# Kernel optimization log

Measured on AMD Instinct MI355X. Metric: run time of the kernel, lower is better.

## Reference

```python
import jax, jax.numpy as jnp
import numpy as np

B, T, F, D, H = 16, 512, 32, 256, 256
EPS = 1e-5


def _layernorm(y, g, b):
    m = jnp.mean(y, axis=-1, keepdims=True)
    v = jnp.mean((y - m) ** 2, axis=-1, keepdims=True)
    return (y - m) / jnp.sqrt(v + EPS) * g + b


def setup_inputs() -> dict:
    key = jax.random.key(0)
    ks = jax.random.split(key, 24)
    s = lambda fan_in: 1.0 / np.sqrt(fan_in)
    u = lambda k, shape, fan_in: jax.random.uniform(k, shape, jnp.float32, -s(fan_in), s(fan_in))
    return {
        "x": jax.random.normal(ks[0], (B, T, F), jnp.float32),
        # per-feature Linear(1, D), stacked over F
        "proj_w": u(ks[1], (F, D), 1),
        "proj_b": u(ks[2], (F, D), 1),
        # per-feature scorer GRN(D, H, 1), stacked over F
        "sc_fc1_w": u(ks[3], (F, H, D), D),
        "sc_fc1_b": u(ks[4], (F, H), D),
        "sc_fc2_w": u(ks[5], (F, 1, H), H),
        "sc_fc2_b": u(ks[6], (F, 1), H),
        "sc_gate_w": u(ks[7], (F, 1, 1), 1),
        "sc_gate_b": u(ks[8], (F, 1), 1),
        "sc_skip_w": u(ks[9], (F, 1, D), D),
        "sc_skip_b": u(ks[10], (F, 1), D),
        "sc_ln_g": jnp.ones((F, 1), jnp.float32),
        "sc_ln_b": jnp.zeros((F, 1), jnp.float32),
        # post GRN(D, H, D); in_dim == out_dim -> skip is identity
        "post_fc1_w": u(ks[11], (H, D), D),
        "post_fc1_b": u(ks[12], (H,), D),
        "post_fc2_w": u(ks[13], (D, H), H),
        "post_fc2_b": u(ks[14], (D,), H),
        "post_gate_w": u(ks[15], (D, D), D),
        "post_gate_b": u(ks[16], (D,), D),
        "post_ln_g": jnp.ones((D,), jnp.float32),
        "post_ln_b": jnp.zeros((D,), jnp.float32),
    }


def reference(x, proj_w, proj_b, sc_fc1_w, sc_fc1_b, sc_fc2_w, sc_fc2_b,
              sc_gate_w, sc_gate_b, sc_skip_w, sc_skip_b, sc_ln_g, sc_ln_b,
              post_fc1_w, post_fc1_b, post_fc2_w, post_fc2_b,
              post_gate_w, post_gate_b, post_ln_g, post_ln_b):
    # per-feature embedding: Linear(1 -> D), batched over F
    # E: [B, T, F, D]
    E = x[..., None] * proj_w[None, None] + proj_b[None, None]

    # per-feature scorer GRN(D, H, 1), all F at once
    h = jax.nn.elu(jnp.einsum("btfd,fhd->btfh", E, sc_fc1_w) + sc_fc1_b)
    h = jnp.einsum("btfh,foh->btfo", h, sc_fc2_w) + sc_fc2_b  # [B,T,F,1]
    g = jax.nn.sigmoid(jnp.einsum("btfo,fpo->btfp", h, sc_gate_w) + sc_gate_b)
    skip = jnp.einsum("btfd,fod->btfo", E, sc_skip_w) + sc_skip_b
    y = g * h + (1.0 - g) * skip
    S = _layernorm(y, sc_ln_g, sc_ln_b)  # [B,T,F,1] (last dim size 1)

    # softmax over features, weighted mixture
    W = jax.nn.softmax(S, axis=2)
    mix = jnp.sum(E * W, axis=2)  # [B,T,D]

    # post GRN(D, H, D), skip = identity
    h2 = jax.nn.elu(mix @ post_fc1_w.T + post_fc1_b)
    h2 = h2 @ post_fc2_w.T + post_fc2_b
    g2 = jax.nn.sigmoid(h2 @ post_gate_w.T + post_gate_b)
    y2 = g2 * h2 + (1.0 - g2) * mix
    return _layernorm(y2, post_ln_g, post_ln_b)
```

## Files before the change

### kernel.cpp

```cpp
#include <hip/hip_runtime.h>
#include <hip/hip_bf16.h>
#include <math.h>


typedef __bf16 bf16;
typedef __bf16 bf16x8 __attribute__((ext_vector_type(8)));
typedef __bf16 bf16x4 __attribute__((ext_vector_type(4)));
typedef float f32x4 __attribute__((ext_vector_type(4)));

#define NTOK 8192
#define D_   256
#define F_   32

#define OFF_C      512
#define OFF_WPROJT 2048
#define OFF_FC1    32768
#define OFF_FC2    163840
#define OFF_GATE   294912

__global__ __launch_bounds__(256) void vsn_prep(
    const float* __restrict__ proj_w, const float* __restrict__ proj_b,
    const float* __restrict__ sc_ln_b,
    const float* __restrict__ w1, const float* __restrict__ w2,
    const float* __restrict__ w3,
    float* __restrict__ wsC, bf16* __restrict__ wsWT,
    bf16* __restrict__ o1, bf16* __restrict__ o2, bf16* __restrict__ o3)
{
  const int blk = blockIdx.x;
  if (blk < 64) {
    int idx = blk * 256 + threadIdx.x;
    {
      float4 a = ((const float4*)w1)[idx];
      bf16x4 b = {(bf16)a.x, (bf16)a.y, (bf16)a.z, (bf16)a.w};
      ((bf16x4*)o1)[idx] = b;
    }
    {
      float4 a = ((const float4*)w2)[idx];
      bf16x4 b = {(bf16)a.x, (bf16)a.y, (bf16)a.z, (bf16)a.w};
      ((bf16x4*)o2)[idx] = b;
    }
    {
      float4 a = ((const float4*)w3)[idx];
      bf16x4 b = {(bf16)a.x, (bf16)a.y, (bf16)a.z, (bf16)a.w};
      ((bf16x4*)o3)[idx] = b;
    }
  } else {
    const int d = threadIdx.x;
    float wv[F_];
    float mx = -3.0e38f;
    #pragma unroll
    for (int f = 0; f < F_; f++) { wv[f] = sc_ln_b[f]; mx = fmaxf(mx, wv[f]); }
    float se = 0.0f;
    #pragma unroll
    for (int f = 0; f < F_; f++) { wv[f] = __expf(wv[f] - mx); se += wv[f]; }
    float inv = 1.0f / se;
    float acc = 0.0f;
    #pragma unroll
    for (int f = 0; f < F_; f++) {
      float wf = wv[f] * inv;
      acc += wf * proj_b[f * D_ + d];
      wsWT[d * F_ + f] = (bf16)(wf * proj_w[f * D_ + d]);
    }
    wsC[d] = acc;
  }
}

__global__ __launch_bounds__(256, 2) void vsn_main(
    const float* __restrict__ x,
    const float* __restrict__ wsC,
    const bf16* __restrict__ WT,
    const bf16* __restrict__ FC1, const float* __restrict__ fc1_b,
    const bf16* __restrict__ FC2, const float* __restrict__ fc2_b,
    const bf16* __restrict__ GATE, const float* __restrict__ gate_b,
    const float* __restrict__ ln_g, const float* __restrict__ ln_b,
    float* __restrict__ out)
{
  __shared__ bf16  sAct[16][264];
  __shared__ float sY[16][260];

  const int tid  = threadIdx.x;
  const int w    = tid >> 6;
  const int lane = tid & 63;
  const int lm   = lane & 15;
  const int lq   = lane >> 4;
  const int j0   = w * 4;
  const int tok0 = blockIdx.x * 16;

  const float* xp = x + (size_t)(tok0 + lm) * F_ + lq * 8;
  float4 x0 = *(const float4*)xp;
  float4 x1 = *(const float4*)(xp + 4);
  bf16x8 a0 = {(bf16)x0.x, (bf16)x0.y, (bf16)x0.z, (bf16)x0.w,
               (bf16)x1.x, (bf16)x1.y, (bf16)x1.z, (bf16)x1.w};
  f32x4 mixf[4];
  #pragma unroll
  for (int jj = 0; jj < 4; jj++) {
    int n = (j0 + jj) * 16 + lm;
    float cv = wsC[n];
    f32x4 acc = {cv, cv, cv, cv};
    bf16x8 b = *(const bf16x8*)(WT + n * F_ + lq * 8);
    acc = __builtin_amdgcn_mfma_f32_16x16x32_bf16(a0, b, acc, 0, 0, 0);
    mixf[jj] = acc;
    #pragma unroll
    for (int r = 0; r < 4; r++) sAct[lq * 4 + r][n] = (bf16)acc[r];
  }
  __syncthreads();

  bf16x8 af[8];
  auto loadA = [&]() {
    #pragma unroll
    for (int ks = 0; ks < 8; ks++)
      af[ks] = *(const bf16x8*)(&sAct[lm][ks * 32 + lq * 8]);
  };
  auto gemmB = [&](const bf16* __restrict__ W, f32x4* acc) {
    bf16x8 bb[8];
    const bf16* wp = W + (size_t)(j0 * 16 + lm) * 256 + lq * 8;
    #pragma unroll
    for (int ks = 0; ks < 8; ks++) bb[ks] = *(const bf16x8*)(wp + ks * 32);
    #pragma unroll
    for (int jj = 0; jj < 4; jj++) {
      bf16x8 bn[8];
      if (jj < 3) {
        const bf16* wn = W + (size_t)((j0 + jj + 1) * 16 + lm) * 256 + lq * 8;
        #pragma unroll
        for (int ks = 0; ks < 8; ks++) bn[ks] = *(const bf16x8*)(wn + ks * 32);
      }
      f32x4 a = {0.f, 0.f, 0.f, 0.f};
      acc[jj] = a;
      #pragma unroll
      for (int ks = 0; ks < 8; ks++)
        acc[jj] = __builtin_amdgcn_mfma_f32_16x16x32_bf16(af[ks], bb[ks], acc[jj], 0, 0, 0);
      if (jj < 3) {
        #pragma unroll
        for (int ks = 0; ks < 8; ks++) bb[ks] = bn[ks];
      }
    }
  };

  loadA();
  __syncthreads();
  {
    f32x4 acc[4];
    gemmB(FC1, acc);
    #pragma unroll
    for (int jj = 0; jj < 4; jj++) {
      int n = (j0 + jj) * 16 + lm;
      float bias = fc1_b[n];
      #pragma unroll
      for (int r = 0; r < 4; r++) {
        float v = acc[jj][r] + bias;
        v = (v > 0.0f) ? v : (__expf(v) - 1.0f);
        sAct[lq * 4 + r][n] = (bf16)v;
      }
    }
  }
  __syncthreads();

  f32x4 h2f[4];
  loadA();
  __syncthreads();
  {
    f32x4 acc[4];
    gemmB(FC2, acc);
    #pragma unroll
    for (int jj = 0; jj < 4; jj++) {
      int n = (j0 + jj) * 16 + lm;
      float bias = fc2_b[n];
      #pragma unroll
      for (int r = 0; r < 4; r++) {
        float v = acc[jj][r] + bias;
        h2f[jj][r] = v;
        sAct[lq * 4 + r][n] = (bf16)v;
      }
    }
  }
  __syncthreads();

  loadA();
  __syncthreads();
  {
    f32x4 acc[4];
    gemmB(GATE, acc);
    #pragma unroll
    for (int jj = 0; jj < 4; jj++) {
      int n = (j0 + jj) * 16 + lm;
      float bias = gate_b[n];
      #pragma unroll
      for (int r = 0; r < 4; r++) {
        float s = acc[jj][r] + bias;
        float g = 1.0f / (1.0f + __expf(-s));
        sY[lq * 4 + r][n] = g * h2f[jj][r] + (1.0f - g) * mixf[jj][r];
      }
    }
  }
  __syncthreads();

  {
    const int t = w * 4 + lq;
    float4 yv[4];
    #pragma unroll
    for (int i = 0; i < 4; i++)
      yv[i] = *(const float4*)(&sY[t][lm * 4 + i * 64]);
    const float inv_d = 1.0f / 256.0f;
    float s = 0.0f;
    #pragma unroll
    for (int i = 0; i < 4; i++) s += yv[i].x + yv[i].y + yv[i].z + yv[i].w;
    #pragma unroll
    for (int off = 1; off < 16; off <<= 1) s += __shfl_xor(s, off);
    float mean = s * inv_d;
    float q = 0.0f;
    #pragma unroll
    for (int i = 0; i < 4; i++) {
      float d0 = yv[i].x - mean, d1 = yv[i].y - mean,
            d2 = yv[i].z - mean, d3 = yv[i].w - mean;
      q += d0 * d0 + d1 * d1 + d2 * d2 + d3 * d3;
    }
    #pragma unroll
    for (int off = 1; off < 16; off <<= 1) q += __shfl_xor(q, off);
    float rstd = rsqrtf(q * inv_d + 1e-5f);
    #pragma unroll
    for (int i = 0; i < 4; i++) {
      int n = lm * 4 + i * 64;
      float4 gv = *(const float4*)(ln_g + n);
      float4 bv = *(const float4*)(ln_b + n);
      float4 o;
      o.x = (yv[i].x - mean) * rstd * gv.x + bv.x;
      o.y = (yv[i].y - mean) * rstd * gv.y + bv.y;
      o.z = (yv[i].z - mean) * rstd * gv.z + bv.z;
      o.w = (yv[i].w - mean) * rstd * gv.w + bv.w;
      *(float4*)(out + (size_t)(tok0 + t) * D_ + n) = o;
    }
  }
}

extern "C" void kernel_launch(void* const* d_in, const int* in_sizes, int n_in,
                              void* d_out, int out_size, void* d_ws, size_t ws_size,
                              hipStream_t stream) {
  (void)in_sizes; (void)n_in; (void)ws_size; (void)out_size;
  const float* x      = (const float*)d_in[0];
  const float* proj_w = (const float*)d_in[1];
  const float* proj_b = (const float*)d_in[2];
  const float* sclnb  = (const float*)d_in[12];
  const float* fc1w   = (const float*)d_in[13];
  const float* fc1b   = (const float*)d_in[14];
  const float* fc2w   = (const float*)d_in[15];
  const float* fc2b   = (const float*)d_in[16];
  const float* gw     = (const float*)d_in[17];
  const float* gb     = (const float*)d_in[18];
  const float* lng    = (const float*)d_in[19];
  const float* lnb    = (const float*)d_in[20];

  char* ws = (char*)d_ws;
  float* wsC   = (float*)(ws + OFF_C);
  bf16*  wsWT  = (bf16*)(ws + OFF_WPROJT);
  bf16*  bFC1  = (bf16*)(ws + OFF_FC1);
  bf16*  bFC2  = (bf16*)(ws + OFF_FC2);
  bf16*  bGATE = (bf16*)(ws + OFF_GATE);

  vsn_prep<<<65, 256, 0, stream>>>(proj_w, proj_b, sclnb, fc1w, fc2w, gw,
                                   wsC, wsWT, bFC1, bFC2, bGATE);
  vsn_main<<<NTOK / 16, 256, 0, stream>>>(x, wsC, wsWT,
                                          bFC1, fc1b, bFC2, fc2b, bGATE, gb,
                                          lng, lnb, (float*)d_out);
}
```

Measured before the change: 126.9 us.

## Process 32 tokens per block with MFMA-swizzled weights and double-buffered LDS

Each main-kernel block now handles 32 tokens instead of 16, so every weight fragment loaded from global memory feeds two MFMAs, which halves the weight traffic per token. The prep kernel rewrites the bf16 weights into a tile-contiguous layout that matches the MFMA fragment order, so the loads are contiguous. A second LDS activation buffer removes the barrier that used to follow each A-fragment load. Mix and h2 values are kept in bf16 registers, which adds some rounding error. The block count drops to 256, which is about one block per CU, and occupancy is lowered to one block per SIMD set, so latency hiding may suffer.

```diff
diff --git a/kernel.cpp b/kernel.cpp
--- a/kernel.cpp
+++ b/kernel.cpp
@@ -17,6 +17,7 @@
 #define OFF_FC1    32768
 #define OFF_FC2    163840
 #define OFF_GATE   294912
+
 
 __global__ __launch_bounds__(256) void vsn_prep(
     const float* __restrict__ proj_w, const float* __restrict__ proj_b,
@@ -27,22 +28,23 @@
     bf16* __restrict__ o1, bf16* __restrict__ o2, bf16* __restrict__ o3)
 {
   const int blk = blockIdx.x;
-  if (blk < 64) {
-    int idx = blk * 256 + threadIdx.x;
-    {
-      float4 a = ((const float4*)w1)[idx];
-      bf16x4 b = {(bf16)a.x, (bf16)a.y, (bf16)a.z, (bf16)a.w};
-      ((bf16x4*)o1)[idx] = b;
-    }
-    {
-      float4 a = ((const float4*)w2)[idx];
-      bf16x4 b = {(bf16)a.x, (bf16)a.y, (bf16)a.z, (bf16)a.w};
-      ((bf16x4*)o2)[idx] = b;
-    }
-    {
-      float4 a = ((const float4*)w3)[idx];
-      bf16x4 b = {(bf16)a.x, (bf16)a.y, (bf16)a.z, (bf16)a.w};
-      ((bf16x4*)o3)[idx] = b;
+  if (blk < 24) {
+    int g = blk * 256 + threadIdx.x;
+    int m = g >> 11;
+    int c = g & 2047;
+    const float* src = (m == 0) ? w1 : (m == 1) ? w2 : w3;
+    bf16* dst = (m == 0) ? o1 : (m == 1) ? o2 : o3;
+    int row = c >> 3, ks = c & 7;
+    int j = row >> 4, lm = row & 15;
+    const float* sp = src + row * 256 + ks * 32;
+    bf16* dp = dst + j * 4096 + ks * 512 + lm * 32;
+    #pragma unroll
+    for (int q = 0; q < 4; q++) {
+      float4 a = ((const float4*)sp)[2 * q];
+      float4 b = ((const float4*)sp)[2 * q + 1];
+      bf16x8 v = {(bf16)a.x, (bf16)a.y, (bf16)a.z, (bf16)a.w,
+                  (bf16)b.x, (bf16)b.y, (bf16)b.z, (bf16)b.w};
+      *(bf16x8*)(dp + q * 8) = v;
     }
   } else {
     const int d = threadIdx.x;
@@ -65,7 +67,7 @@
   }
 }
 
-__global__ __launch_bounds__(256, 2) void vsn_main(
+__global__ __launch_bounds__(256, 1) void vsn_main(
     const float* __restrict__ x,
     const float* __restrict__ wsC,
     const bf16* __restrict__ WT,
@@ -75,8 +77,8 @@
     const float* __restrict__ ln_g, const float* __restrict__ ln_b,
     float* __restrict__ out)
 {
-  __shared__ bf16  sAct[16][264];
-  __shared__ float sY[16][260];
+  __shared__ bf16  sAct[2][32][264];
+  __shared__ float sY[32][260];
 
   const int tid  = threadIdx.x;
   const int w    = tid >> 6;
@@ -84,51 +86,66 @@
   const int lm   = lane & 15;
   const int lq   = lane >> 4;
   const int j0   = w * 4;
-  const int tok0 = blockIdx.x * 16;
-
-  const float* xp = x + (size_t)(tok0 + lm) * F_ + lq * 8;
-  float4 x0 = *(const float4*)xp;
-  float4 x1 = *(const float4*)(xp + 4);
-  bf16x8 a0 = {(bf16)x0.x, (bf16)x0.y, (bf16)x0.z, (bf16)x0.w,
-               (bf16)x1.x, (bf16)x1.y, (bf16)x1.z, (bf16)x1.w};
-  f32x4 mixf[4];
-  #pragma unroll
-  for (int jj = 0; jj < 4; jj++) {
-    int n = (j0 + jj) * 16 + lm;
-    float cv = wsC[n];
-    f32x4 acc = {cv, cv, cv, cv};
-    bf16x8 b = *(const bf16x8*)(WT + n * F_ + lq * 8);
-    acc = __builtin_amdgcn_mfma_f32_16x16x32_bf16(a0, b, acc, 0, 0, 0);
-    mixf[jj] = acc;
-    #pragma unroll
-    for (int r = 0; r < 4; r++) sAct[lq * 4 + r][n] = (bf16)acc[r];
+  const int tok0 = blockIdx.x * 32;
+
+  bf16x4 mixh[2][4];
+  {
+    bf16x8 a[2];
+    #pragma unroll
+    for (int t = 0; t < 2; t++) {
+      const float* xp = x + (size_t)(tok0 + t * 16 + lm) * F_ + lq * 8;
+      float4 x0 = *(const float4*)xp;
+      float4 x1 = *(const float4*)(xp + 4);
+      bf16x8 av = {(bf16)x0.x, (bf16)x0.y, (bf16)x0.z, (bf16)x0.w,
+                   (bf16)x1.x, (bf16)x1.y, (bf16)x1.z, (bf16)x1.w};
+      a[t] = av;
+    }
+    #pragma unroll
+    for (int jj = 0; jj < 4; jj++) {
+      int n = (j0 + jj) * 16 + lm;
+      bf16x8 b = *(const bf16x8*)(WT + n * F_ + lq * 8);
+      float cv = wsC[n];
+      #pragma unroll
+      for (int t = 0; t < 2; t++) {
+        f32x4 acc = {cv, cv, cv, cv};
+        acc = __builtin_amdgcn_mfma_f32_16x16x32_bf16(a[t], b, acc, 0, 0, 0);
+        bf16x4 mh = {(bf16)acc[0], (bf16)acc[1], (bf16)acc[2], (bf16)acc[3]};
+        mixh[t][jj] = mh;
+        #pragma unroll
+        for (int r = 0; r < 4; r++) sAct[0][t * 16 + lq * 4 + r][n] = mh[r];
+      }
+    }
   }
   __syncthreads();
 
-  bf16x8 af[8];
-  auto loadA = [&]() {
+  auto gemmPhase = [&](int src, const bf16* __restrict__ W, auto&& epi) {
+    bf16x8 af[2][8];
+    #pragma unroll
+    for (int t = 0; t < 2; t++)
+      #pragma unroll
+      for (int ks = 0; ks < 8; ks++)
+        af[t][ks] = *(const bf16x8*)(&sAct[src][t * 16 + lm][ks * 32 + lq * 8]);
+    const bf16* base = W + j0 * 4096 + lm * 32 + lq * 8;
+    bf16x8 bb[8];
     #pragma unroll
     for (int ks = 0; ks < 8; ks++)
-      af[ks] = *(const bf16x8*)(&sAct[lm][ks * 32 + lq * 8]);
-  };
-  auto gemmB = [&](const bf16* __restrict__ W, f32x4* acc) {
-    bf16x8 bb[8];
-    const bf16* wp = W + (size_t)(j0 * 16 + lm) * 256 + lq * 8;
-    #pragma unroll
-    for (int ks = 0; ks < 8; ks++) bb[ks] = *(const bf16x8*)(wp + ks * 32);
+      bb[ks] = *(const bf16x8*)(base + ks * 512);
     #pragma unroll
     for (int jj = 0; jj < 4; jj++) {
       bf16x8 bn[8];
       if (jj < 3) {
-        const bf16* wn = W + (size_t)((j0 + jj + 1) * 16 + lm) * 256 + lq * 8;
+        const bf16* nb = base + (jj + 1) * 4096;
         #pragma unroll
-        for (int ks = 0; ks < 8; ks++) bn[ks] = *(const bf16x8*)(wn + ks * 32);
-      }
-      f32x4 a = {0.f, 0.f, 0.f, 0.f};
-      acc[jj] = a;
+        for (int ks = 0; ks < 8; ks++)
+          bn[ks] = *(const bf16x8*)(nb + ks * 512);
+      }
+      f32x4 acc0 = {0.f, 0.f, 0.f, 0.f}, acc1 = {0.f, 0.f, 0.f, 0.f};
       #pragma unroll
-      for (int ks = 0; ks < 8; ks++)
-        acc[jj] = __builtin_amdgcn_mfma_f32_16x16x32_bf16(af[ks], bb[ks], acc[jj], 0, 0, 0);
+      for (int ks = 0; ks < 8; ks++) {
+        acc0 = __builtin_amdgcn_mfma_f32_16x16x32_bf16(af[0][ks], bb[ks], acc0, 0, 0, 0);
+        acc1 = __builtin_amdgcn_mfma_f32_16x16x32_bf16(af[1][ks], bb[ks], acc1, 0, 0, 0);
+      }
+      epi(jj, acc0, acc1);
       if (jj < 3) {
         #pragma unroll
         for (int ks = 0; ks < 8; ks++) bb[ks] = bn[ks];
@@ -136,71 +153,61 @@
     }
   };
 
-  loadA();
-  __syncthreads();
-  {
-    f32x4 acc[4];
-    gemmB(FC1, acc);
-    #pragma unroll
-    for (int jj = 0; jj < 4; jj++) {
-      int n = (j0 + jj) * 16 + lm;
-      float bias = fc1_b[n];
-      #pragma unroll
-      for (int r = 0; r < 4; r++) {
-        float v = acc[jj][r] + bias;
-        v = (v > 0.0f) ? v : (__expf(v) - 1.0f);
-        sAct[lq * 4 + r][n] = (bf16)v;
-      }
-    }
-  }
-  __syncthreads();
-
-  f32x4 h2f[4];
-  loadA();
-  __syncthreads();
-  {
-    f32x4 acc[4];
-    gemmB(FC2, acc);
-    #pragma unroll
-    for (int jj = 0; jj < 4; jj++) {
-      int n = (j0 + jj) * 16 + lm;
-      float bias = fc2_b[n];
-      #pragma unroll
-      for (int r = 0; r < 4; r++) {
-        float v = acc[jj][r] + bias;
-        h2f[jj][r] = v;
-        sAct[lq * 4 + r][n] = (bf16)v;
-      }
-    }
-  }
-  __syncthreads();
-
-  loadA();
-  __syncthreads();
-  {
-    f32x4 acc[4];
-    gemmB(GATE, acc);
-    #pragma unroll
-    for (int jj = 0; jj < 4; jj++) {
-      int n = (j0 + jj) * 16 + lm;
-      float bias = gate_b[n];
-      #pragma unroll
-      for (int r = 0; r < 4; r++) {
-        float s = acc[jj][r] + bias;
-        float g = 1.0f / (1.0f + __expf(-s));
-        sY[lq * 4 + r][n] = g * h2f[jj][r] + (1.0f - g) * mixf[jj][r];
-      }
-    }
-  }
-  __syncthreads();
-
-  {
-    const int t = w * 4 + lq;
+  gemmPhase(0, FC1, [&](int jj, f32x4& a0, f32x4& a1) {
+    int n = (j0 + jj) * 16 + lm;
+    float bias = fc1_b[n];
+    #pragma unroll
+    for (int r = 0; r < 4; r++) {
+      float v0 = a0[r] + bias;
+      v0 = (v0 > 0.0f) ? v0 : (__expf(v0) - 1.0f);
+      sAct[1][lq * 4 + r][n] = (bf16)v0;
+      float v1 = a1[r] + bias;
+      v1 = (v1 > 0.0f) ? v1 : (__expf(v1) - 1.0f);
+      sAct[1][16 + lq * 4 + r][n] = (bf16)v1;
+    }
+  });
+  __syncthreads();
+
+  bf16x4 h2h[2][4];
+  gemmPhase(1, FC2, [&](int jj, f32x4& a0, f32x4& a1) {
+    int n = (j0 + jj) * 16 + lm;
+    float bias = fc2_b[n];
+    bf16x4 h0, h1v;
+    #pragma unroll
+    for (int r = 0; r < 4; r++) {
+      h0[r]  = (bf16)(a0[r] + bias);
+      h1v[r] = (bf16)(a1[r] + bias);
+      sAct[0][lq * 4 + r][n] = h0[r];
+      sAct[0][16 + lq * 4 + r][n] = h1v[r];
+    }
+    h2h[0][jj] = h0;
+    h2h[1][jj] = h1v;
+  });
+  __syncthreads();
+
+  gemmPhase(0, GATE, [&](int jj, f32x4& a0, f32x4& a1) {
+    int n = (j0 + jj) * 16 + lm;
+    float bias = gate_b[n];
+    #pragma unroll
+    for (int r = 0; r < 4; r++) {
+      float s0 = a0[r] + bias;
+      float g0 = 1.0f / (1.0f + __expf(-s0));
+      sY[lq * 4 + r][n] = g0 * (float)h2h[0][jj][r] + (1.0f - g0) * (float)mixh[0][jj][r];
+      float s1 = a1[r] + bias;
+      float g1 = 1.0f / (1.0f + __expf(-s1));
+      sY[16 + lq * 4 + r][n] = g1 * (float)h2h[1][jj][r] + (1.0f - g1) * (float)mixh[1][jj][r];
+    }
+  });
+  __syncthreads();
+
+  const float inv_d = 1.0f / 256.0f;
+  #pragma unroll
+  for (int rep = 0; rep < 2; rep++) {
+    const int t = (w * 4 + lq) * 2 + rep;
     float4 yv[4];
     #pragma unroll
     for (int i = 0; i < 4; i++)
       yv[i] = *(const float4*)(&sY[t][lm * 4 + i * 64]);
-    const float inv_d = 1.0f / 256.0f;
     float s = 0.0f;
     #pragma unroll
     for (int i = 0; i < 4; i++) s += yv[i].x + yv[i].y + yv[i].z + yv[i].w;
@@ -256,9 +263,9 @@
   bf16*  bFC2  = (bf16*)(ws + OFF_FC2);
   bf16*  bGATE = (bf16*)(ws + OFF_GATE);
 
-  vsn_prep<<<65, 256, 0, stream>>>(proj_w, proj_b, sclnb, fc1w, fc2w, gw,
+  vsn_prep<<<25, 256, 0, stream>>>(proj_w, proj_b, sclnb, fc1w, fc2w, gw,
                                    wsC, wsWT, bFC1, bFC2, bGATE);
-  vsn_main<<<NTOK / 16, 256, 0, stream>>>(x, wsC, wsWT,
+  vsn_main<<<NTOK / 32, 256, 0, stream>>>(x, wsC, wsWT,
                                           bFC1, fc1b, bFC2, fc2b, bGATE, gb,
                                           lng, lnb, (float*)d_out);
 }
```

Measured after the change: 113.4 us. -10.6%, faster.

## Pre-tile bf16 weights for MFMA fragments, double-buffer LDS, fuse LayerNorm in registers

Applied to the files above, without the earlier changes.

The prep kernel now writes the bf16 weight matrices in a tiled order that matches the MFMA B-fragment layout, so each lane's eight bf16x8 loads per tile fall in one contiguous 4 KB block instead of striding across 256-element rows. The main kernel uses two LDS activation buffers so phases can read one while writing the other, which removes the extra barriers around each A-fragment load. LayerNorm is computed straight from the gate-phase accumulators using sum and sum-of-squares with a small cross-wave LDS reduction, which removes the fp32 staging tile. mix and h2 are now kept as bf16 in registers, which lowers register pressure but adds rounding error to the residual, and the single-pass variance formula is less numerically stable.

```diff
diff --git a/kernel.cpp b/kernel.cpp
--- a/kernel.cpp
+++ b/kernel.cpp
@@ -17,6 +17,7 @@
 #define OFF_FC1    32768
 #define OFF_FC2    163840
 #define OFF_GATE   294912
+
 
 __global__ __launch_bounds__(256) void vsn_prep(
     const float* __restrict__ proj_w, const float* __restrict__ proj_b,
@@ -27,22 +28,23 @@
     bf16* __restrict__ o1, bf16* __restrict__ o2, bf16* __restrict__ o3)
 {
   const int blk = blockIdx.x;
-  if (blk < 64) {
-    int idx = blk * 256 + threadIdx.x;
-    {
-      float4 a = ((const float4*)w1)[idx];
-      bf16x4 b = {(bf16)a.x, (bf16)a.y, (bf16)a.z, (bf16)a.w};
-      ((bf16x4*)o1)[idx] = b;
-    }
-    {
-      float4 a = ((const float4*)w2)[idx];
-      bf16x4 b = {(bf16)a.x, (bf16)a.y, (bf16)a.z, (bf16)a.w};
-      ((bf16x4*)o2)[idx] = b;
-    }
-    {
-      float4 a = ((const float4*)w3)[idx];
-      bf16x4 b = {(bf16)a.x, (bf16)a.y, (bf16)a.z, (bf16)a.w};
-      ((bf16x4*)o3)[idx] = b;
+  if (blk < 24) {
+    int g = blk * 256 + threadIdx.x;
+    int m = g >> 11;
+    int c = g & 2047;
+    const float* src = (m == 0) ? w1 : (m == 1) ? w2 : w3;
+    bf16* dst = (m == 0) ? o1 : (m == 1) ? o2 : o3;
+    int row = c >> 3, ks = c & 7;
+    int j = row >> 4, lm = row & 15;
+    const float* sp = src + row * 256 + ks * 32;
+    bf16* dp = dst + j * 4096 + ks * 512 + lm * 32;
+    #pragma unroll
+    for (int q = 0; q < 4; q++) {
+      float4 a = ((const float4*)sp)[2 * q];
+      float4 b = ((const float4*)sp)[2 * q + 1];
+      bf16x8 v = {(bf16)a.x, (bf16)a.y, (bf16)a.z, (bf16)a.w,
+                  (bf16)b.x, (bf16)b.y, (bf16)b.z, (bf16)b.w};
+      *(bf16x8*)(dp + q * 8) = v;
     }
   } else {
     const int d = threadIdx.x;
@@ -75,8 +77,8 @@
     const float* __restrict__ ln_g, const float* __restrict__ ln_b,
     float* __restrict__ out)
 {
-  __shared__ bf16  sAct[16][264];
-  __shared__ float sY[16][260];
+  __shared__ bf16  sAct[2][16][264];
+  __shared__ float sLN[4][16][2];
 
   const int tid  = threadIdx.x;
   const int w    = tid >> 6;
@@ -86,43 +88,46 @@
   const int j0   = w * 4;
   const int tok0 = blockIdx.x * 16;
 
-  const float* xp = x + (size_t)(tok0 + lm) * F_ + lq * 8;
-  float4 x0 = *(const float4*)xp;
-  float4 x1 = *(const float4*)(xp + 4);
-  bf16x8 a0 = {(bf16)x0.x, (bf16)x0.y, (bf16)x0.z, (bf16)x0.w,
-               (bf16)x1.x, (bf16)x1.y, (bf16)x1.z, (bf16)x1.w};
-  f32x4 mixf[4];
-  #pragma unroll
-  for (int jj = 0; jj < 4; jj++) {
-    int n = (j0 + jj) * 16 + lm;
-    float cv = wsC[n];
-    f32x4 acc = {cv, cv, cv, cv};
-    bf16x8 b = *(const bf16x8*)(WT + n * F_ + lq * 8);
-    acc = __builtin_amdgcn_mfma_f32_16x16x32_bf16(a0, b, acc, 0, 0, 0);
-    mixf[jj] = acc;
-    #pragma unroll
-    for (int r = 0; r < 4; r++) sAct[lq * 4 + r][n] = (bf16)acc[r];
-  }
-  __syncthreads();
-
-  bf16x8 af[8];
-  auto loadA = [&]() {
+  bf16x4 mixh[4];
+  {
+    const float* xp = x + (size_t)(tok0 + lm) * F_ + lq * 8;
+    float4 x0 = *(const float4*)xp;
+    float4 x1 = *(const float4*)(xp + 4);
+    bf16x8 a0 = {(bf16)x0.x, (bf16)x0.y, (bf16)x0.z, (bf16)x0.w,
+                 (bf16)x1.x, (bf16)x1.y, (bf16)x1.z, (bf16)x1.w};
+    #pragma unroll
+    for (int jj = 0; jj < 4; jj++) {
+      int n = (j0 + jj) * 16 + lm;
+      bf16x8 b = *(const bf16x8*)(WT + n * F_ + lq * 8);
+      float cv = wsC[n];
+      f32x4 acc = {cv, cv, cv, cv};
+      acc = __builtin_amdgcn_mfma_f32_16x16x32_bf16(a0, b, acc, 0, 0, 0);
+      bf16x4 mh = {(bf16)acc[0], (bf16)acc[1], (bf16)acc[2], (bf16)acc[3]};
+      mixh[jj] = mh;
+      #pragma unroll
+      for (int r = 0; r < 4; r++) sAct[0][lq * 4 + r][n] = mh[r];
+    }
+  }
+  __syncthreads();
+
+  auto gemmPhase = [&](int src, const bf16* __restrict__ W, f32x4* acc) {
+    bf16x8 af[8];
     #pragma unroll
     for (int ks = 0; ks < 8; ks++)
-      af[ks] = *(const bf16x8*)(&sAct[lm][ks * 32 + lq * 8]);
-  };
-  auto gemmB = [&](const bf16* __restrict__ W, f32x4* acc) {
+      af[ks] = *(const bf16x8*)(&sAct[src][lm][ks * 32 + lq * 8]);
+    const bf16* base = W + j0 * 4096 + lm * 32 + lq * 8;
     bf16x8 bb[8];
-    const bf16* wp = W + (size_t)(j0 * 16 + lm) * 256 + lq * 8;
-    #pragma unroll
-    for (int ks = 0; ks < 8; ks++) bb[ks] = *(const bf16x8*)(wp + ks * 32);
+    #pragma unroll
+    for (int ks = 0; ks < 8; ks++)
+      bb[ks] = *(const bf16x8*)(base + ks * 512);
     #pragma unroll
     for (int jj = 0; jj < 4; jj++) {
       bf16x8 bn[8];
       if (jj < 3) {
-        const bf16* wn = W + (size_t)((j0 + jj + 1) * 16 + lm) * 256 + lq * 8;
+        const bf16* nb = base + (jj + 1) * 4096;
         #pragma unroll
-        for (int ks = 0; ks < 8; ks++) bn[ks] = *(const bf16x8*)(wn + ks * 32);
+        for (int ks = 0; ks < 8; ks++)
+          bn[ks] = *(const bf16x8*)(nb + ks * 512);
       }
       f32x4 a = {0.f, 0.f, 0.f, 0.f};
       acc[jj] = a;
@@ -136,11 +141,9 @@
     }
   };
 
-  loadA();
-  __syncthreads();
   {
     f32x4 acc[4];
-    gemmB(FC1, acc);
+    gemmPhase(0, FC1, acc);
     #pragma unroll
     for (int jj = 0; jj < 4; jj++) {
       int n = (j0 + jj) * 16 + lm;
@@ -149,85 +152,85 @@
       for (int r = 0; r < 4; r++) {
         float v = acc[jj][r] + bias;
         v = (v > 0.0f) ? v : (__expf(v) - 1.0f);
-        sAct[lq * 4 + r][n] = (bf16)v;
-      }
-    }
-  }
-  __syncthreads();
-
-  f32x4 h2f[4];
-  loadA();
-  __syncthreads();
+        sAct[1][lq * 4 + r][n] = (bf16)v;
+      }
+    }
+  }
+  __syncthreads();
+
+  bf16x4 h2h[4];
   {
     f32x4 acc[4];
-    gemmB(FC2, acc);
+    gemmPhase(1, FC2, acc);
     #pragma unroll
     for (int jj = 0; jj < 4; jj++) {
       int n = (j0 + jj) * 16 + lm;
       float bias = fc2_b[n];
+      bf16x4 hh;
       #pragma unroll
       for (int r = 0; r < 4; r++) {
-        float v = acc[jj][r] + bias;
-        h2f[jj][r] = v;
-        sAct[lq * 4 + r][n] = (bf16)v;
-      }
-    }
-  }
-  __syncthreads();
-
-  loadA();
-  __syncthreads();
-  {
-    f32x4 acc[4];
-    gemmB(GATE, acc);
-    #pragma unroll
-    for (int jj = 0; jj < 4; jj++) {
-      int n = (j0 + jj) * 16 + lm;
-      float bias = gate_b[n];
-      #pragma unroll
-      for (int r = 0; r < 4; r++) {
-        float s = acc[jj][r] + bias;
-        float g = 1.0f / (1.0f + __expf(-s));
-        sY[lq * 4 + r][n] = g * h2f[jj][r] + (1.0f - g) * mixf[jj][r];
-      }
-    }
-  }
-  __syncthreads();
-
-  {
-    const int t = w * 4 + lq;
-    float4 yv[4];
-    #pragma unroll
-    for (int i = 0; i < 4; i++)
-      yv[i] = *(const float4*)(&sY[t][lm * 4 + i * 64]);
-    const float inv_d = 1.0f / 256.0f;
-    float s = 0.0f;
-    #pragma unroll
-    for (int i = 0; i < 4; i++) s += yv[i].x + yv[i].y + yv[i].z + yv[i].w;
-    #pragma unroll
-    for (int off = 1; off < 16; off <<= 1) s += __shfl_xor(s, off);
-    float mean = s * inv_d;
-    float q = 0.0f;
-    #pragma unroll
-    for (int i = 0; i < 4; i++) {
-      float d0 = yv[i].x - mean, d1 = yv[i].y - mean,
-            d2 = yv[i].z - mean, d3 = yv[i].w - mean;
-      q += d0 * d0 + d1 * d1 + d2 * d2 + d3 * d3;
-    }
-    #pragma unroll
-    for (int off = 1; off < 16; off <<= 1) q += __shfl_xor(q, off);
-    float rstd = rsqrtf(q * inv_d + 1e-5f);
-    #pragma unroll
-    for (int i = 0; i < 4; i++) {
-      int n = lm * 4 + i * 64;
-      float4 gv = *(const float4*)(ln_g + n);
-      float4 bv = *(const float4*)(ln_b + n);
-      float4 o;
-      o.x = (yv[i].x - mean) * rstd * gv.x + bv.x;
-      o.y = (yv[i].y - mean) * rstd * gv.y + bv.y;
-      o.z = (yv[i].z - mean) * rstd * gv.z + bv.z;
-      o.w = (yv[i].w - mean) * rstd * gv.w + bv.w;
-      *(float4*)(out + (size_t)(tok0 + t) * D_ + n) = o;
+        hh[r] = (bf16)(acc[jj][r] + bias);
+        sAct[0][lq * 4 + r][n] = hh[r];
+      }
+      h2h[jj] = hh;
+    }
+  }
+  __syncthreads();
+
+  f32x4 acc4[4];
+  gemmPhase(0, GATE, acc4);
+  float rs[4] = {0.f, 0.f, 0.f, 0.f}, rq[4] = {0.f, 0.f, 0.f, 0.f};
+  #pragma unroll
+  for (int jj = 0; jj < 4; jj++) {
+    int n = (j0 + jj) * 16 + lm;
+    float bias = gate_b[n];
+    #pragma unroll
+    for (int r = 0; r < 4; r++) {
+      float s = acc4[jj][r] + bias;
+      float g = 1.0f / (1.0f + __expf(-s));
+      float y = g * (float)h2h[jj][r] + (1.0f - g) * (float)mixh[jj][r];
+      acc4[jj][r] = y;
+      rs[r] += y;
+      rq[r] += y * y;
+    }
+  }
+
+  #pragma unroll
+  for (int r = 0; r < 4; r++) {
+    #pragma unroll
+    for (int off = 1; off < 16; off <<= 1) {
+      rs[r] += __shfl_xor(rs[r], off);
+      rq[r] += __shfl_xor(rq[r], off);
+    }
+  }
+  if (lm == 0) {
+    #pragma unroll
+    for (int r = 0; r < 4; r++) {
+      sLN[w][lq * 4 + r][0] = rs[r];
+      sLN[w][lq * 4 + r][1] = rq[r];
+    }
+  }
+  __syncthreads();
+
+  const float inv_d = 1.0f / 256.0f;
+  float mean[4], rstd[4];
+  #pragma unroll
+  for (int r = 0; r < 4; r++) {
+    int row = lq * 4 + r;
+    float S = sLN[0][row][0] + sLN[1][row][0] + sLN[2][row][0] + sLN[3][row][0];
+    float Q = sLN[0][row][1] + sLN[1][row][1] + sLN[2][row][1] + sLN[3][row][1];
+    float m = S * inv_d;
+    mean[r] = m;
+    rstd[r] = rsqrtf(Q * inv_d - m * m + 1e-5f);
+  }
+  #pragma unroll
+  for (int jj = 0; jj < 4; jj++) {
+    int n = (j0 + jj) * 16 + lm;
+    float lg = ln_g[n], lb = ln_b[n];
+    #pragma unroll
+    for (int r = 0; r < 4; r++) {
+      float o = (acc4[jj][r] - mean[r]) * rstd[r] * lg + lb;
+      out[(size_t)(tok0 + lq * 4 + r) * D_ + n] = o;
     }
   }
 }
@@ -256,7 +259,7 @@
   bf16*  bFC2  = (bf16*)(ws + OFF_FC2);
   bf16*  bGATE = (bf16*)(ws + OFF_GATE);
 
-  vsn_prep<<<65, 256, 0, stream>>>(proj_w, proj_b, sclnb, fc1w, fc2w, gw,
+  vsn_prep<<<25, 256, 0, stream>>>(proj_w, proj_b, sclnb, fc1w, fc2w, gw,
                                    wsC, wsWT, bFC1, bFC2, bGATE);
   vsn_main<<<NTOK / 16, 256, 0, stream>>>(x, wsC, wsWT,
                                           bFC1, fc1b, bFC2, fc2b, bGATE, gb,
```

Result: faster. 121.3 us (-4.4%).
